# Optimization experiments

Hardware: AMD Instinct MI355X
Metric: run time of the kernel (lower is better)

The kernel has to match this reference:

```python
import jax, jax.numpy as jnp
import numpy as np
from jax import lax

B, C, H, W = 32, 4, 84, 84
A, N, D = 8, 20000, 128
P = 50          # kNN neighbors used by each DND
DELTA = 1e-3    # inverse-distance kernel delta


def _conv(x, w, stride):
    return lax.conv_general_dilated(
        x, w, window_strides=(stride, stride), padding='VALID',
        dimension_numbers=('NCHW', 'OIHW', 'NCHW'))


def embed(states, conv1_w, conv1_b, conv2_w, conv2_b, conv3_w, conv3_b, fc_w, fc_b):
    x = jax.nn.relu(_conv(states, conv1_w, 4) + conv1_b[None, :, None, None])  # [B,32,20,20]
    x = jax.nn.relu(_conv(x, conv2_w, 2) + conv2_b[None, :, None, None])       # [B,64,9,9]
    x = jax.nn.relu(_conv(x, conv3_w, 1) + conv3_b[None, :, None, None])       # [B,64,7,7]
    x = x.reshape(x.shape[0], -1)                                              # [B,3136]
    return x @ fc_w.T + fc_b                                                   # [B,128] keys


def setup_inputs() -> dict:
    key = jax.random.key(0)
    ks = jax.random.split(key, 9)
    sc = lambda fan_in: 1.0 / np.sqrt(fan_in)
    return {
        'states': jax.random.normal(ks[0], (B, C, H, W), jnp.float32),
        'actions': jax.random.randint(ks[1], (B,), 0, A, jnp.int64 if jax.config.jax_enable_x64 else jnp.int32),
        'conv1_w': jax.random.normal(ks[2], (32, 4, 8, 8), jnp.float32) * sc(4 * 64),
        'conv1_b': jnp.zeros((32,), jnp.float32),
        'conv2_w': jax.random.normal(ks[3], (64, 32, 4, 4), jnp.float32) * sc(32 * 16),
        'conv2_b': jnp.zeros((64,), jnp.float32),
        'conv3_w': jax.random.normal(ks[4], (64, 64, 3, 3), jnp.float32) * sc(64 * 9),
        'conv3_b': jnp.zeros((64,), jnp.float32),
        'fc_w': jax.random.normal(ks[5], (D, 3136), jnp.float32) * sc(3136),
        'fc_b': jnp.zeros((D,), jnp.float32),
        'dnd_keys': jax.random.normal(ks[6], (A, N, D), jnp.float32),
        'dnd_values': jax.random.normal(ks[7], (A, N), jnp.float32),
    }


def reference(states, actions, conv1_w, conv1_b, conv2_w, conv2_b, conv3_w, conv3_b,
              fc_w, fc_b, dnd_keys, dnd_values):
    h = embed(states, conv1_w, conv1_b, conv2_w, conv2_b, conv3_w, conv3_b, fc_w, fc_b)  # [B,D]
    # Route each sample to its action's DND memory (batched gather).
    tab_k = dnd_keys[actions]    # [B,N,D]
    tab_v = dnd_values[actions]  # [B,N]
    # Squared L2 distances via expansion (avoids [B,N,D] diff intermediate).
    d2 = (jnp.sum(h * h, -1)[:, None]
          - 2.0 * jnp.einsum('bd,bnd->bn', h, tab_k)
          + jnp.sum(tab_k * tab_k, -1))  # [B,N]
    neg_top, idx = lax.top_k(-d2, P)     # P nearest neighbors per sample
    top_d2 = jnp.maximum(-neg_top, 0.0)
    w = 1.0 / (top_d2 + DELTA)           # inverse-distance kernel
    w = w / jnp.sum(w, -1, keepdims=True)
    v = jnp.take_along_axis(tab_v, idx, axis=1)  # [B,P]
    q = jnp.sum(w * v, -1)               # [B]
    return q
```

## Files before the change

kernel.cpp:

```cpp
#include <hip/hip_runtime.h>

#define BB 32
#define AA 8
#define NN 20000
#define DD 128
#define PP 50
#define DELTA 1e-3f

typedef unsigned long long ull;

__global__ __launch_bounds__(256) void conv1_k(const float* __restrict__ x,
                                               const float* __restrict__ w,
                                               const float* __restrict__ bias,
                                               float* __restrict__ y) {
    int idx = blockIdx.x * 256 + threadIdx.x;
    if (idx >= 32 * 32 * 20 * 20) return;
    int ox = idx % 20;
    int t = idx / 20;
    int oy = t % 20; t /= 20;
    int oc = t % 32;
    int b = t / 32;
    float acc = bias[oc];
    const float* xb = x + (size_t)b * 4 * 84 * 84;
    const float* wk = w + oc * 4 * 64;
    for (int ic = 0; ic < 4; ic++) {
        const float* xc = xb + ic * 84 * 84 + (oy * 4) * 84 + ox * 4;
        const float* wc = wk + ic * 64;
#pragma unroll
        for (int ky = 0; ky < 8; ky++) {
            const float4* xr = (const float4*)(xc + ky * 84);
            const float4* wr = (const float4*)(wc + ky * 8);
            float4 x0 = xr[0], x1 = xr[1];
            float4 w0 = wr[0], w1 = wr[1];
            acc += x0.x * w0.x + x0.y * w0.y + x0.z * w0.z + x0.w * w0.w
                 + x1.x * w1.x + x1.y * w1.y + x1.z * w1.z + x1.w * w1.w;
        }
    }
    y[idx] = fmaxf(acc, 0.f);
}

__global__ __launch_bounds__(256) void conv2_k(const float* __restrict__ x,
                                               const float* __restrict__ w,
                                               const float* __restrict__ bias,
                                               float* __restrict__ y) {
    int idx = blockIdx.x * 256 + threadIdx.x;
    if (idx >= 32 * 64 * 9 * 9) return;
    int ox = idx % 9;
    int t = idx / 9;
    int oy = t % 9; t /= 9;
    int oc = t % 64;
    int b = t / 64;
    float acc = bias[oc];
    const float* xb = x + (size_t)b * 32 * 400;
    const float* wk = w + oc * 32 * 16;
    for (int ic = 0; ic < 32; ic++) {
        const float* xc = xb + ic * 400 + (oy * 2) * 20 + ox * 2;
        const float* wc = wk + ic * 16;
#pragma unroll
        for (int ky = 0; ky < 4; ky++) {
            const float2* xr = (const float2*)(xc + ky * 20);
            float2 x0 = xr[0], x1 = xr[1];
            float4 wv = ((const float4*)(wc + ky * 4))[0];
            acc += x0.x * wv.x + x0.y * wv.y + x1.x * wv.z + x1.y * wv.w;
        }
    }
    y[idx] = fmaxf(acc, 0.f);
}

__global__ __launch_bounds__(256) void conv3_k(const float* __restrict__ x,
                                               const float* __restrict__ w,
                                               const float* __restrict__ bias,
                                               float* __restrict__ y) {
    int idx = blockIdx.x * 256 + threadIdx.x;
    if (idx >= 32 * 64 * 7 * 7) return;
    int ox = idx % 7;
    int t = idx / 7;
    int oy = t % 7; t /= 7;
    int oc = t % 64;
    int b = t / 64;
    float acc = bias[oc];
    const float* xb = x + (size_t)b * 64 * 81;
    const float* wk = w + oc * 64 * 9;
    for (int ic = 0; ic < 64; ic++) {
        const float* xc = xb + ic * 81 + oy * 9 + ox;
        const float* wc = wk + ic * 9;
#pragma unroll
        for (int ky = 0; ky < 3; ky++)
#pragma unroll
            for (int kx = 0; kx < 3; kx++)
                acc += xc[ky * 9 + kx] * wc[ky * 3 + kx];
    }
    y[idx] = fmaxf(acc, 0.f);
}

__global__ __launch_bounds__(256) void fc_k(const float* __restrict__ x,
                                            const float* __restrict__ w,
                                            const float* __restrict__ bias,
                                            float* __restrict__ h) {
    __shared__ float sx[3136];
    int b = blockIdx.x >> 3;
    int g = blockIdx.x & 7;
    int tid = threadIdx.x;
    const float4* xr = (const float4*)(x + (size_t)b * 3136);
    float4* sx4w = (float4*)sx;
    for (int i = tid; i < 784; i += 256) sx4w[i] = xr[i];
    __syncthreads();
    int oc_local = tid >> 4;
    int kslice = tid & 15;
    int oc = g * 16 + oc_local;
    const float4* wr = (const float4*)(w + (size_t)oc * 3136);
    const float4* sx4 = (const float4*)sx;
    float acc = 0.f;
#pragma unroll 7
    for (int j = 0; j < 49; j++) {
        int i = kslice + 16 * j;
        float4 a = sx4[i], c = wr[i];
        acc += a.x * c.x + a.y * c.y + a.z * c.z + a.w * c.w;
    }
#pragma unroll
    for (int m = 8; m >= 1; m >>= 1) acc += __shfl_xor(acc, m);
    if (kslice == 0) h[b * 128 + oc] = acc + bias[oc];
}

__global__ __launch_bounds__(256) void dist4_k(const float* __restrict__ h,
                                               const int* __restrict__ actions,
                                               const float* __restrict__ keys,
                                               float* __restrict__ d2) {
    int a = blockIdx.y;
    int tid = threadIdx.x;
    int lane = tid & 63, wave = tid >> 6;
    __shared__ float4 tile[64 * 32];
    __shared__ float4 hl4[BB * 32];
    __shared__ int sl[BB];
    __shared__ int s_m;

    if (wave == 0) {
        int act = (lane < BB) ? actions[lane] : -1;
        ull mask = __ballot(act == a);
        if (act == a) {
            int pos = __popcll(mask & ((1ull << lane) - 1));
            sl[pos] = lane;
        }
        if (lane == 0) s_m = __popcll(mask);
    }
    __syncthreads();
    int m = s_m;
    if (m == 0) return;

    for (int i = tid; i < m * 32; i += 256) {
        int s = i >> 5, g = i & 31;
        hl4[i] = ((const float4*)(h + sl[s] * DD))[g];
    }

    int r0 = blockIdx.x * 64;
    int valid = min(64, NN - r0);
    const float4* kb4 = (const float4*)(keys + (size_t)a * NN * DD);
#pragma unroll
    for (int i = 0; i < 8; i++) {
        int idx = i * 256 + tid;
        int row = idx >> 5, g = idx & 31;
        if (row < valid)
            tile[row * 32 + ((g + (row & 31)) & 31)] = kb4[(size_t)(r0 + row) * 32 + g];
    }
    __syncthreads();

    int row = lane;
    if (row < valid) {
        int c = row & 31;
        const float4* trow = &tile[row * 32];
        for (int s = wave; s < m; s += 4) {
            const float4* hp = &hl4[s * 32];
            float acc = 0.f;
#pragma unroll 8
            for (int g = 0; g < 32; g++) {
                float4 kv = trow[(g + c) & 31];
                float4 hv = hp[g];
                float dx = hv.x - kv.x, dy = hv.y - kv.y;
                float dz = hv.z - kv.z, dw = hv.w - kv.w;
                acc += dx * dx + dy * dy + dz * dz + dw * dw;
            }
            d2[(size_t)sl[s] * NN + r0 + row] = acc;
        }
    }
}

__global__ __launch_bounds__(1024) void select_k(const float* __restrict__ d2,
                                                 const float* __restrict__ values,
                                                 const int* __restrict__ actions,
                                                 float* __restrict__ q) {
    const int NB = 8160;
    const int CAP = 512;
    int b = blockIdx.x, tid = threadIdx.x;
    int lane = tid & 63, wave = tid >> 6;
    __shared__ int hist[NB];
    __shared__ int fhist[1024];
    __shared__ float cd[CAP];
    __shared__ int ci[CAP];
    __shared__ int scounter;
    __shared__ int s_t, s_below;
    __shared__ int s_ft;
    __shared__ int wsum[16];
    __shared__ float rw[16], rwv[16];

    const float* db = d2 + (size_t)b * NN;
    for (int i = tid; i < NB; i += 1024) hist[i] = 0;
    fhist[tid] = 0;
    if (tid == 0) scounter = 0;
    __syncthreads();

    for (int i = tid; i < NN; i += 1024)
        atomicAdd(&hist[__float_as_uint(db[i]) >> 18], 1);
    __syncthreads();

    {
        int s = 0;
#pragma unroll
        for (int u = 0; u < 8; u++) s += hist[tid * 8 + u];
        int sc = s;
#pragma unroll
        for (int m = 1; m < 64; m <<= 1) {
            int o = __shfl_up(sc, m);
            if (lane >= m) sc += o;
        }
        if (lane == 63) wsum[wave] = sc;
        __syncthreads();
        if (tid < 16) {
            int vc = wsum[tid];
            for (int m = 1; m < 16; m <<= 1) {
                int o = __shfl_up(vc, m);
                if (tid >= m) vc += o;
            }
            wsum[tid] = vc;
        }
        __syncthreads();
        int incl = ((wave == 0) ? 0 : wsum[wave - 1]) + sc;
        int excl = incl - s;
        if (excl < PP && incl >= PP) {
            int c = excl;
#pragma unroll
            for (int u = 0; u < 8; u++) {
                int bkt = tid * 8 + u;
                int hv = hist[bkt];
                if (c < PP && c + hv >= PP) { s_t = bkt; s_below = c; }
                c += hv;
            }
        }
    }
    __syncthreads();
    int t = s_t, below = s_below;

    for (int i = tid; i < NN; i += 1024) {
        unsigned bits = __float_as_uint(db[i]);
        if ((int)(bits >> 18) == t) atomicAdd(&fhist[(bits >> 8) & 1023], 1);
    }
    __syncthreads();

    {
        int s = fhist[tid];
        int sc = s;
#pragma unroll
        for (int m = 1; m < 64; m <<= 1) {
            int o = __shfl_up(sc, m);
            if (lane >= m) sc += o;
        }
        if (lane == 63) wsum[wave] = sc;
        __syncthreads();
        if (tid < 16) {
            int vc = wsum[tid];
            for (int m = 1; m < 16; m <<= 1) {
                int o = __shfl_up(vc, m);
                if (tid >= m) vc += o;
            }
            wsum[tid] = vc;
        }
        __syncthreads();
        int incl = ((wave == 0) ? 0 : wsum[wave - 1]) + sc;
        int excl = incl - s;
        if (below + excl < PP && below + incl >= PP) s_ft = tid;
    }
    __syncthreads();
    int ft = s_ft;

    for (int i = tid; i < NN; i += 1024) {
        unsigned bits = __float_as_uint(db[i]);
        int c = (int)(bits >> 18);
        bool take = (c < t) || (c == t && (int)((bits >> 8) & 1023) <= ft);
        if (take) {
            int slot = atomicAdd(&scounter, 1);
            if (slot < CAP) { cd[slot] = db[i]; ci[slot] = i; }
        }
    }
    __syncthreads();
    int k = min(scounter, CAP);

    float w = 0.f, wv = 0.f;
    int a = actions[b];
    for (int s = tid; s < k; s += 1024) {
        ull key = ((ull)__float_as_uint(cd[s]) << 32) | (unsigned)ci[s];
        int cnt = 0;
        for (int j = 0; j < k; j++) {
            ull kj = ((ull)__float_as_uint(cd[j]) << 32) | (unsigned)ci[j];
            cnt += (kj < key);
        }
        if (cnt < PP) {
            float dd = fmaxf(cd[s], 0.f);
            float ww = 1.f / (dd + DELTA);
            w += ww;
            wv += ww * values[(size_t)a * NN + ci[s]];
        }
    }
#pragma unroll
    for (int m = 32; m >= 1; m >>= 1) {
        w += __shfl_xor(w, m);
        wv += __shfl_xor(wv, m);
    }
    if (lane == 0) { rw[wave] = w; rwv[wave] = wv; }
    __syncthreads();
    if (tid < 16) {
        float tw = rw[tid], twv = rwv[tid];
#pragma unroll
        for (int m = 8; m >= 1; m >>= 1) {
            tw += __shfl_xor(tw, m);
            twv += __shfl_xor(twv, m);
        }
        if (tid == 0) q[b] = twv / tw;
    }
}

extern "C" void kernel_launch(void* const* d_in, const int* in_sizes, int n_in,
                              void* d_out, int out_size, void* d_ws, size_t ws_size,
                              hipStream_t stream) {
    const float* states = (const float*)d_in[0];
    const int* actions = (const int*)d_in[1];
    const float* c1w = (const float*)d_in[2];
    const float* c1b = (const float*)d_in[3];
    const float* c2w = (const float*)d_in[4];
    const float* c2b = (const float*)d_in[5];
    const float* c3w = (const float*)d_in[6];
    const float* c3b = (const float*)d_in[7];
    const float* fcw = (const float*)d_in[8];
    const float* fcb = (const float*)d_in[9];
    const float* keys = (const float*)d_in[10];
    const float* vals = (const float*)d_in[11];
    float* out = (float*)d_out;

    float* ws = (float*)d_ws;
    float* c1o = ws;
    float* c2o = c1o + 409600;
    float* c3o = c2o + 165888;
    float* h   = c3o + 100352;
    float* d2  = h + 4096;

    conv1_k<<<(409600 + 255) / 256, 256, 0, stream>>>(states, c1w, c1b, c1o);
    conv2_k<<<(165888 + 255) / 256, 256, 0, stream>>>(c1o, c2w, c2b, c2o);
    conv3_k<<<(100352 + 255) / 256, 256, 0, stream>>>(c2o, c3w, c3b, c3o);
    fc_k<<<256, 256, 0, stream>>>(c3o, fcw, fcb, h);
    dist4_k<<<dim3(313, AA), 256, 0, stream>>>(h, actions, keys, d2);
    select_k<<<BB, 1024, 0, stream>>>(d2, vals, actions, out);
}
```

Before: 251.1 us.

## Tile conv layers per sample and output-channel group with shared-memory staging

```diff
diff --git a/kernel.cpp b/kernel.cpp
--- a/kernel.cpp
+++ b/kernel.cpp
@@ -13,84 +13,135 @@
                                                const float* __restrict__ w,
                                                const float* __restrict__ bias,
                                                float* __restrict__ y) {
-    int idx = blockIdx.x * 256 + threadIdx.x;
-    if (idx >= 32 * 32 * 20 * 20) return;
-    int ox = idx % 20;
-    int t = idx / 20;
-    int oy = t % 20; t /= 20;
-    int oc = t % 32;
-    int b = t / 32;
-    float acc = bias[oc];
+    int b = blockIdx.x >> 2;
+    int og = blockIdx.x & 3;
+    int tid = threadIdx.x;
+    __shared__ __align__(16) float wl[8 * 256];
+    {
+        const float4* wg = (const float4*)(w + og * 2048);
+        float4* wl4 = (float4*)wl;
+        for (int i = tid; i < 512; i += 256) wl4[i] = wg[i];
+    }
+    float bb[8];
+#pragma unroll
+    for (int o = 0; o < 8; o++) bb[o] = bias[og * 8 + o];
+    __syncthreads();
+
     const float* xb = x + (size_t)b * 4 * 84 * 84;
-    const float* wk = w + oc * 4 * 64;
-    for (int ic = 0; ic < 4; ic++) {
-        const float* xc = xb + ic * 84 * 84 + (oy * 4) * 84 + ox * 4;
-        const float* wc = wk + ic * 64;
-#pragma unroll
-        for (int ky = 0; ky < 8; ky++) {
-            const float4* xr = (const float4*)(xc + ky * 84);
-            const float4* wr = (const float4*)(wc + ky * 8);
-            float4 x0 = xr[0], x1 = xr[1];
-            float4 w0 = wr[0], w1 = wr[1];
-            acc += x0.x * w0.x + x0.y * w0.y + x0.z * w0.z + x0.w * w0.w
-                 + x1.x * w1.x + x1.y * w1.y + x1.z * w1.z + x1.w * w1.w;
-        }
-    }
-    y[idx] = fmaxf(acc, 0.f);
+    for (int pp = tid; pp < 400; pp += 256) {
+        int oy = pp / 20, ox = pp % 20;
+        float acc[8];
+#pragma unroll
+        for (int o = 0; o < 8; o++) acc[o] = bb[o];
+        for (int ic = 0; ic < 4; ic++) {
+            const float* xc = xb + ic * 7056 + (oy * 4) * 84 + ox * 4;
+#pragma unroll
+            for (int ky = 0; ky < 8; ky++) {
+                const float4* xr = (const float4*)(xc + ky * 84);
+                float4 x0 = xr[0], x1 = xr[1];
+                float xv[8] = {x0.x, x0.y, x0.z, x0.w, x1.x, x1.y, x1.z, x1.w};
+                const float* wrow = wl + ic * 64 + ky * 8;
+#pragma unroll
+                for (int o = 0; o < 8; o++) {
+                    const float* wo = wrow + o * 256;
+#pragma unroll
+                    for (int kx = 0; kx < 8; kx++) acc[o] += xv[kx] * wo[kx];
+                }
+            }
+        }
+#pragma unroll
+        for (int o = 0; o < 8; o++)
+            y[((size_t)(b * 32 + og * 8 + o)) * 400 + pp] = fmaxf(acc[o], 0.f);
+    }
 }
 
 __global__ __launch_bounds__(256) void conv2_k(const float* __restrict__ x,
                                                const float* __restrict__ w,
                                                const float* __restrict__ bias,
                                                float* __restrict__ y) {
-    int idx = blockIdx.x * 256 + threadIdx.x;
-    if (idx >= 32 * 64 * 9 * 9) return;
-    int ox = idx % 9;
-    int t = idx / 9;
-    int oy = t % 9; t /= 9;
-    int oc = t % 64;
-    int b = t / 64;
-    float acc = bias[oc];
-    const float* xb = x + (size_t)b * 32 * 400;
-    const float* wk = w + oc * 32 * 16;
-    for (int ic = 0; ic < 32; ic++) {
-        const float* xc = xb + ic * 400 + (oy * 2) * 20 + ox * 2;
-        const float* wc = wk + ic * 16;
-#pragma unroll
-        for (int ky = 0; ky < 4; ky++) {
-            const float2* xr = (const float2*)(xc + ky * 20);
-            float2 x0 = xr[0], x1 = xr[1];
-            float4 wv = ((const float4*)(wc + ky * 4))[0];
-            acc += x0.x * wv.x + x0.y * wv.y + x1.x * wv.z + x1.y * wv.w;
-        }
-    }
-    y[idx] = fmaxf(acc, 0.f);
+    int b = blockIdx.x >> 3;
+    int og = blockIdx.x & 7;
+    int tid = threadIdx.x;
+    __shared__ __align__(16) float xs[12800];
+    __shared__ __align__(16) float ws[8 * 512];
+    {
+        const float4* xg = (const float4*)(x + (size_t)b * 12800);
+        float4* xs4 = (float4*)xs;
+        for (int i = tid; i < 3200; i += 256) xs4[i] = xg[i];
+        const float4* wg = (const float4*)(w + og * 4096);
+        float4* ws4 = (float4*)ws;
+        for (int i = tid; i < 1024; i += 256) ws4[i] = wg[i];
+    }
+    __syncthreads();
+
+    if (tid < 162) {
+        int pos = tid >> 1, half = tid & 1;
+        int oy = pos / 9, ox = pos % 9;
+        float acc[4];
+#pragma unroll
+        for (int o = 0; o < 4; o++) acc[o] = bias[og * 8 + half * 4 + o];
+        for (int ic = 0; ic < 32; ic++) {
+            const float* xrow = xs + ic * 400 + (oy * 2) * 20 + ox * 2;
+#pragma unroll
+            for (int ky = 0; ky < 4; ky++) {
+                float x0 = xrow[ky * 20], x1 = xrow[ky * 20 + 1];
+                float x2 = xrow[ky * 20 + 2], x3 = xrow[ky * 20 + 3];
+                const float* wrow = ws + (half * 4) * 512 + ic * 16 + ky * 4;
+#pragma unroll
+                for (int o = 0; o < 4; o++) {
+                    const float* wo = wrow + o * 512;
+                    acc[o] += x0 * wo[0] + x1 * wo[1] + x2 * wo[2] + x3 * wo[3];
+                }
+            }
+        }
+#pragma unroll
+        for (int o = 0; o < 4; o++)
+            y[((size_t)(b * 64 + og * 8 + half * 4 + o)) * 81 + pos] = fmaxf(acc[o], 0.f);
+    }
 }
 
 __global__ __launch_bounds__(256) void conv3_k(const float* __restrict__ x,
                                                const float* __restrict__ w,
                                                const float* __restrict__ bias,
                                                float* __restrict__ y) {
-    int idx = blockIdx.x * 256 + threadIdx.x;
-    if (idx >= 32 * 64 * 7 * 7) return;
-    int ox = idx % 7;
-    int t = idx / 7;
-    int oy = t % 7; t /= 7;
-    int oc = t % 64;
-    int b = t / 64;
-    float acc = bias[oc];
-    const float* xb = x + (size_t)b * 64 * 81;
-    const float* wk = w + oc * 64 * 9;
-    for (int ic = 0; ic < 64; ic++) {
-        const float* xc = xb + ic * 81 + oy * 9 + ox;
-        const float* wc = wk + ic * 9;
-#pragma unroll
-        for (int ky = 0; ky < 3; ky++)
-#pragma unroll
-            for (int kx = 0; kx < 3; kx++)
-                acc += xc[ky * 9 + kx] * wc[ky * 3 + kx];
-    }
-    y[idx] = fmaxf(acc, 0.f);
+    int b = blockIdx.x >> 3;
+    int og = blockIdx.x & 7;
+    int tid = threadIdx.x;
+    __shared__ __align__(16) float xs[5184];
+    __shared__ __align__(16) float ws[8 * 576];
+    {
+        const float4* xg = (const float4*)(x + (size_t)b * 5184);
+        float4* xs4 = (float4*)xs;
+        for (int i = tid; i < 1296; i += 256) xs4[i] = xg[i];
+        const float4* wg = (const float4*)(w + og * 4608);
+        float4* ws4 = (float4*)ws;
+        for (int i = tid; i < 1152; i += 256) ws4[i] = wg[i];
+    }
+    __syncthreads();
+
+    if (tid < 196) {
+        int pos = tid >> 2, q = tid & 3;
+        int oy = pos / 7, ox = pos % 7;
+        float acc[2];
+#pragma unroll
+        for (int o = 0; o < 2; o++) acc[o] = bias[og * 8 + q * 2 + o];
+        for (int ic = 0; ic < 64; ic++) {
+            const float* xrow = xs + ic * 81 + oy * 9 + ox;
+#pragma unroll
+            for (int ky = 0; ky < 3; ky++) {
+                float x0 = xrow[ky * 9], x1 = xrow[ky * 9 + 1], x2 = xrow[ky * 9 + 2];
+                const float* wrow = ws + (q * 2) * 576 + ic * 9 + ky * 3;
+#pragma unroll
+                for (int o = 0; o < 2; o++) {
+                    const float* wo = wrow + o * 576;
+                    acc[o] += x0 * wo[0] + x1 * wo[1] + x2 * wo[2];
+                }
+            }
+        }
+#pragma unroll
+        for (int o = 0; o < 2; o++)
+            y[((size_t)(b * 64 + og * 8 + q * 2 + o)) * 49 + pos] = fmaxf(acc[o], 0.f);
+    }
 }
 
 __global__ __launch_bounds__(256) void fc_k(const float* __restrict__ x,
@@ -351,9 +402,9 @@
     float* h   = c3o + 100352;
     float* d2  = h + 4096;
 
-    conv1_k<<<(409600 + 255) / 256, 256, 0, stream>>>(states, c1w, c1b, c1o);
-    conv2_k<<<(165888 + 255) / 256, 256, 0, stream>>>(c1o, c2w, c2b, c2o);
-    conv3_k<<<(100352 + 255) / 256, 256, 0, stream>>>(c2o, c3w, c3b, c3o);
+    conv1_k<<<128, 256, 0, stream>>>(states, c1w, c1b, c1o);
+    conv2_k<<<256, 256, 0, stream>>>(c1o, c2w, c2b, c2o);
+    conv3_k<<<256, 256, 0, stream>>>(c2o, c3w, c3b, c3o);
     fc_k<<<256, 256, 0, stream>>>(c3o, fcw, fcb, h);
     dist4_k<<<dim3(313, AA), 256, 0, stream>>>(h, actions, keys, d2);
     select_k<<<BB, 1024, 0, stream>>>(d2, vals, actions, out);
```

New measurement: 248.5 us. Within noise of the previous version (-1.0%).
